# Optimization experiments

Hardware: AMD Instinct MI355X
Metric: run time of the kernel (lower is better)

Reference implementation:

```python
import jax, jax.numpy as jnp
import numpy as np

L, T, D, H, NC = 4, 2, 128, 8, 7
DH = D // H
DFF = 4 * D
EPS = 1e-5


def _ln(x, w, b):
    m = jnp.mean(x, axis=-1, keepdims=True)
    v = jnp.mean((x - m) ** 2, axis=-1, keepdims=True)
    return (x - m) / jnp.sqrt(v + EPS) * w + b


def setup_inputs() -> dict:
    key = jax.random.key(0)
    ks = jax.random.split(key, 16)
    s = 0.02
    inp = {
        "x": jax.random.normal(ks[0], (65536, 1, 2 * D), dtype=jnp.float32),
        "token_proj_w": jax.random.normal(ks[1], (T * D, T * D), dtype=jnp.float32) * s,
        "token_proj_b": jnp.zeros((T * D,), jnp.float32),
        "pos_emb": jax.random.normal(ks[2], (1, T, D), dtype=jnp.float32),
        "qkv_w": jax.random.normal(ks[3], (L, 3 * D, D), dtype=jnp.float32) * s,
        "qkv_b": jnp.zeros((L, 3 * D), jnp.float32),
        "out_w": jax.random.normal(ks[4], (L, D, D), dtype=jnp.float32) * s,
        "out_b": jnp.zeros((L, D), jnp.float32),
        "ln1_w": jnp.ones((L, D), jnp.float32),
        "ln1_b": jnp.zeros((L, D), jnp.float32),
        "ff1_w": jax.random.normal(ks[5], (L, DFF, D), dtype=jnp.float32) * s,
        "ff1_b": jnp.zeros((L, DFF), jnp.float32),
        "ff2_w": jax.random.normal(ks[6], (L, D, DFF), dtype=jnp.float32) * s,
        "ff2_b": jnp.zeros((L, D), jnp.float32),
        "ln2_w": jnp.ones((L, D), jnp.float32),
        "ln2_b": jnp.zeros((L, D), jnp.float32),
        "lnf_w": jnp.ones((D,), jnp.float32),
        "lnf_b": jnp.zeros((D,), jnp.float32),
        "cls_ln_w": jnp.ones((D,), jnp.float32),
        "cls_ln_b": jnp.zeros((D,), jnp.float32),
        "cls_w": jax.random.normal(ks[7], (NC, D), dtype=jnp.float32) * s,
        "cls_b": jnp.zeros((NC,), jnp.float32),
    }
    return inp


def _forward(x, token_proj_w, token_proj_b, pos_emb, qkv_w, qkv_b, out_w, out_b,
             ln1_w, ln1_b, ff1_w, ff1_b, ff2_w, ff2_b, ln2_w, ln2_b,
             lnf_w, lnf_b, cls_ln_w, cls_ln_b, cls_w, cls_b):
    x = jnp.squeeze(x, 1)                                  # [B, 256]
    B = x.shape[0]
    tok = x @ token_proj_w.T + token_proj_b                # [B, 256]
    tok = tok.reshape(B, T, D) + pos_emb                   # [B, 2, 128]
    scale = 1.0 / jnp.sqrt(jnp.float32(DH))
    for i in range(L):
        # --- self-attention (post-norm, as in nn.TransformerEncoderLayer) ---
        qkv = jnp.einsum('btd,ed->bte', tok, qkv_w[i]) + qkv_b[i]   # [B,T,3D]
        q, k, v = jnp.split(qkv, 3, axis=-1)
        q = q.reshape(B, T, H, DH)
        k = k.reshape(B, T, H, DH)
        v = v.reshape(B, T, H, DH)
        scores = jnp.einsum('bqhd,bkhd->bhqk', q, k) * scale
        attn = jax.nn.softmax(scores, axis=-1)
        o = jnp.einsum('bhqk,bkhd->bqhd', attn, v).reshape(B, T, D)
        o = jnp.einsum('btd,ed->bte', o, out_w[i]) + out_b[i]
        tok = _ln(tok + o, ln1_w[i], ln1_b[i])
        # --- FFN ---
        h = jnp.einsum('btd,fd->btf', tok, ff1_w[i]) + ff1_b[i]
        h = jax.nn.gelu(h, approximate=False)
        h = jnp.einsum('btf,df->btd', h, ff2_w[i]) + ff2_b[i]
        tok = _ln(tok + h, ln2_w[i], ln2_b[i])
    tok = _ln(tok, lnf_w, lnf_b)                           # final encoder norm
    pooled = jnp.mean(tok, axis=1)                         # [B, D]
    out = _ln(pooled, cls_ln_w, cls_ln_b)
    out = jax.nn.gelu(out, approximate=False)
    return out @ cls_w.T + cls_b                           # [B, 7]


def reference(x, token_proj_w, token_proj_b, pos_emb, qkv_w, qkv_b, out_w, out_b,
              ln1_w, ln1_b, ff1_w, ff1_b, ff2_w, ff2_b, ln2_w, ln2_b,
              lnf_w, lnf_b, cls_ln_w, cls_ln_b, cls_w, cls_b):
    return _forward(x, token_proj_w, token_proj_b, pos_emb, qkv_w, qkv_b, out_w, out_b,
                    ln1_w, ln1_b, ff1_w, ff1_b, ff2_w, ff2_b, ln2_w, ln2_b,
                    lnf_w, lnf_b, cls_ln_w, cls_ln_b, cls_w, cls_b)
```

## Files before the change

kernel.cpp:

```cpp
#include <hip/hip_runtime.h>


#define DEV static __device__ __forceinline__

typedef __attribute__((ext_vector_type(8))) short short8;
typedef __attribute__((ext_vector_type(4))) float f32x4;

#define BS    32
#define MROWS 64
#define PITCH 136
#define XP    272
#define LEPS  1e-5f

#define OFF_TPW  0
#define OFF_QKVW 65536
#define OFF_OUTW 262144
#define OFF_FF1W 327680
#define OFF_FF2W 589824
#define WS_ELEMS 851968

DEV unsigned short f2b(float f) {
  unsigned u = __float_as_uint(f);
  return (unsigned short)((u + 0x7fffu + ((u >> 16) & 1u)) >> 16);
}
DEV float b2f(unsigned short s) { return __uint_as_float((unsigned)s << 16); }

DEV f32x4 MFMA(short8 a, short8 b, f32x4 c) {
  return __builtin_amdgcn_mfma_f32_16x16x32_bf16(a, b, c, 0, 0, 0);
}

DEV float gelu_f(float x) {
  float u = 0.7978845608028654f * (x + 0.044715f * x * x * x);
  float e = __expf(2.0f * u);
  float t = 1.0f - 2.0f / (e + 1.0f);
  return 0.5f * x * (1.0f + t);
}

DEV short8 ldfrag(const unsigned short* tile, int rowBase, int kk, int lane) {
  return *(const short8*)(tile + (rowBase + (lane & 15)) * PITCH + kk * 32 + (lane >> 4) * 8);
}
DEV short8 ldfragX(const unsigned short* tile, int rowBase, int koff, int lane) {
  return *(const short8*)(tile + (rowBase + (lane & 15)) * XP + koff + (lane >> 4) * 8);
}
DEV short8 ldBg(const unsigned short* __restrict__ base, int pitch, int colBase,
                int koff, int kk, int lane) {
  return *(const short8*)(base + (size_t)(colBase + (lane & 15)) * pitch +
                          koff + kk * 32 + (lane >> 4) * 8);
}

DEV void ln_residual_write(f32x4 (&val)[2][4], const float* __restrict__ w,
                           const float* __restrict__ b, unsigned short* sTok,
                           float* sRedP, float* sRedF, int tid) {
  const int wave = tid >> 6, lane = tid & 63, g = lane >> 4, j = lane & 15;
  float ps[4][4], pq[4][4];
#pragma unroll
  for (int rt = 0; rt < 4; ++rt)
#pragma unroll
    for (int r = 0; r < 4; ++r) {
      float v0 = val[0][rt][r], v1 = val[1][rt][r];
      float s = v0 + v1, q = v0 * v0 + v1 * v1;
#pragma unroll
      for (int m = 1; m < 16; m <<= 1) {
        s += __shfl_xor(s, m, 16);
        q += __shfl_xor(q, m, 16);
      }
      ps[rt][r] = s; pq[rt][r] = q;
    }
  if (j == 0) {
#pragma unroll
    for (int rt = 0; rt < 4; ++rt)
#pragma unroll
      for (int r = 0; r < 4; ++r) {
        int row = rt * 16 + g * 4 + r;
        sRedP[row * 8 + wave * 2]     = ps[rt][r];
        sRedP[row * 8 + wave * 2 + 1] = pq[rt][r];
      }
  }
  __syncthreads();
  if (tid < 64) {
    float s = 0.f, q = 0.f;
#pragma unroll
    for (int wv = 0; wv < 4; ++wv) {
      s += sRedP[tid * 8 + wv * 2];
      q += sRedP[tid * 8 + wv * 2 + 1];
    }
    float mean = s * (1.f / 128.f);
    sRedF[tid * 2]     = mean;
    sRedF[tid * 2 + 1] = rsqrtf(q * (1.f / 128.f) - mean * mean + LEPS);
  }
  __syncthreads();
#pragma unroll
  for (int h = 0; h < 2; ++h) {
    int n = (h * 4 + wave) * 16 + j;
    float wn = w[n], bn = b[n];
#pragma unroll
    for (int rt = 0; rt < 4; ++rt)
#pragma unroll
      for (int r = 0; r < 4; ++r) {
        int row = rt * 16 + g * 4 + r;
        float mean = sRedF[row * 2], rstd = sRedF[row * 2 + 1];
        sTok[row * PITCH + n] = f2b((val[h][rt][r] - mean) * rstd * wn + bn);
      }
  }
  __syncthreads();
}

__global__ __launch_bounds__(256)
void prep_w(const float* __restrict__ tpw, const float* __restrict__ qkvw,
            const float* __restrict__ outw, const float* __restrict__ ff1w,
            const float* __restrict__ ff2w, unsigned short* __restrict__ wsb) {
  int i = blockIdx.x * 256 + threadIdx.x;
  if (i >= WS_ELEMS) return;
  float v;
  if (i < OFF_QKVW)      v = tpw[i - OFF_TPW];
  else if (i < OFF_OUTW) v = qkvw[i - OFF_QKVW];
  else if (i < OFF_FF1W) v = outw[i - OFF_OUTW];
  else if (i < OFF_FF2W) v = ff1w[i - OFF_FF1W];
  else                   v = ff2w[i - OFF_FF2W];
  wsb[i] = f2b(v);
}

__global__ __launch_bounds__(256, 2)
void tx_fused(const float* __restrict__ x, const unsigned short* __restrict__ wsb,
              const float* __restrict__ tpb, const float* __restrict__ pos,
              const float* __restrict__ qkvb, const float* __restrict__ outb,
              const float* __restrict__ ln1w, const float* __restrict__ ln1b,
              const float* __restrict__ ff1b, const float* __restrict__ ff2b,
              const float* __restrict__ ln2w, const float* __restrict__ ln2b,
              const float* __restrict__ lnfw, const float* __restrict__ lnfb,
              const float* __restrict__ clnw, const float* __restrict__ clnb,
              const float* __restrict__ cw, const float* __restrict__ cb,
              float* __restrict__ out) {
  __shared__ __align__(16) unsigned short sTok[MROWS * PITCH];
  __shared__ __align__(16) unsigned short sStage[MROWS * PITCH];
  __shared__ float sRedP[MROWS * 8];
  __shared__ float sRedF[MROWS * 2];

  const int tid  = threadIdx.x;
  const int wave = tid >> 6;
  const int lane = tid & 63;
  const int g = lane >> 4, j = lane & 15;
  const size_t s0 = (size_t)blockIdx.x * BS;

  const unsigned short* tpwB  = wsb + OFF_TPW;
  const unsigned short* qkvwB = wsb + OFF_QKVW;
  const unsigned short* outwB = wsb + OFF_OUTW;
  const unsigned short* ff1wB = wsb + OFF_FF1W;
  const unsigned short* ff2wB = wsb + OFF_FF2W;

  const f32x4 zero4 = {0.f, 0.f, 0.f, 0.f};

  {
#pragma unroll
    for (int it = 0; it < 2; ++it) {
      int idx = it * 256 + tid;
      int r = idx >> 4, s = idx & 15;
      const float4* p = (const float4*)(x + (s0 + r) * 256 + s * 16);
      float4 f0 = p[0], f1 = p[1], f2 = p[2], f3 = p[3];
      short8 lo, hi;
      lo[0] = (short)f2b(f0.x); lo[1] = (short)f2b(f0.y);
      lo[2] = (short)f2b(f0.z); lo[3] = (short)f2b(f0.w);
      lo[4] = (short)f2b(f1.x); lo[5] = (short)f2b(f1.y);
      lo[6] = (short)f2b(f1.z); lo[7] = (short)f2b(f1.w);
      hi[0] = (short)f2b(f2.x); hi[1] = (short)f2b(f2.y);
      hi[2] = (short)f2b(f2.z); hi[3] = (short)f2b(f2.w);
      hi[4] = (short)f2b(f3.x); hi[5] = (short)f2b(f3.y);
      hi[6] = (short)f2b(f3.z); hi[7] = (short)f2b(f3.w);
      *(short8*)(sStage + r * XP + s * 16)     = lo;
      *(short8*)(sStage + r * XP + s * 16 + 8) = hi;
    }
  }
  __syncthreads();

  f32x4 accTP[2][2][2];
#pragma unroll
  for (int nc = 0; nc < 2; ++nc)
#pragma unroll
    for (int h = 0; h < 2; ++h)
#pragma unroll
      for (int rt = 0; rt < 2; ++rt) accTP[nc][h][rt] = zero4;

#pragma unroll
  for (int kc = 0; kc < 2; ++kc)
#pragma unroll
    for (int nc = 0; nc < 2; ++nc)
#pragma unroll
      for (int h = 0; h < 2; ++h) {
        int cb = nc * 128 + (h * 4 + wave) * 16;
        short8 bf[4];
#pragma unroll
        for (int kk = 0; kk < 4; ++kk)
          bf[kk] = ldBg(tpwB, 256, cb, kc * 128, kk, lane);
#pragma unroll
        for (int rt = 0; rt < 2; ++rt)
#pragma unroll
          for (int kk = 0; kk < 4; ++kk)
            accTP[nc][h][rt] = MFMA(ldfragX(sStage, rt * 16, kc * 128 + kk * 32, lane),
                                    bf[kk], accTP[nc][h][rt]);
      }
  __syncthreads();
#pragma unroll
  for (int nc = 0; nc < 2; ++nc)
#pragma unroll
    for (int h = 0; h < 2; ++h) {
      int d = (h * 4 + wave) * 16 + j;
      float bias = tpb[nc * 128 + d] + pos[nc * 128 + d];
#pragma unroll
      for (int rt = 0; rt < 2; ++rt)
#pragma unroll
        for (int r = 0; r < 4; ++r) {
          int sm = rt * 16 + g * 4 + r;
          sTok[(2 * sm + nc) * PITCH + d] = f2b(accTP[nc][h][rt][r] + bias);
        }
    }
  __syncthreads();

  for (int li = 0; li < 4; ++li) {
    const unsigned short* qkvL = qkvwB + (size_t)li * 49152;
    const unsigned short* outL = outwB + (size_t)li * 16384;
    const unsigned short* ff1L = ff1wB + (size_t)li * 65536;
    const unsigned short* ff2L = ff2wB + (size_t)li * 65536;

    short8 aT[4][4];
#pragma unroll
    for (int rt = 0; rt < 4; ++rt)
#pragma unroll
      for (int kk = 0; kk < 4; ++kk) aT[rt][kk] = ldfrag(sTok, rt * 16, kk, lane);

    f32x4 acc[6][4];
#pragma unroll
    for (int a = 0; a < 6; ++a)
#pragma unroll
      for (int rt = 0; rt < 4; ++rt) acc[a][rt] = zero4;

#pragma unroll
    for (int nc = 0; nc < 3; ++nc)
#pragma unroll
      for (int h = 0; h < 2; ++h) {
        int cb = nc * 128 + (h * 4 + wave) * 16;
        short8 bf[4];
#pragma unroll
        for (int kk = 0; kk < 4; ++kk) bf[kk] = ldBg(qkvL, 128, cb, 0, kk, lane);
        int a = nc * 2 + h;
#pragma unroll
        for (int rt = 0; rt < 4; ++rt)
#pragma unroll
          for (int kk = 0; kk < 4; ++kk)
            acc[a][rt] = MFMA(aT[rt][kk], bf[kk], acc[a][rt]);
      }
#pragma unroll
    for (int a = 0; a < 6; ++a) {
      int nc = a >> 1, h = a & 1;
      float bv = qkvb[li * 384 + nc * 128 + (h * 4 + wave) * 16 + j];
#pragma unroll
      for (int rt = 0; rt < 4; ++rt) acc[a][rt] += bv;
    }

#pragma unroll
    for (int hh = 0; hh < 2; ++hh) {
      int head = hh * 4 + wave;
#pragma unroll
      for (int rt = 0; rt < 4; ++rt)
#pragma unroll
        for (int sp = 0; sp < 2; ++sp) {
          int r0 = sp * 2, r1 = r0 + 1;
          float q0 = acc[hh][rt][r0],     q1 = acc[hh][rt][r1];
          float k0 = acc[2 + hh][rt][r0], k1 = acc[2 + hh][rt][r1];
          float s00 = q0 * k0, s01 = q0 * k1, s10 = q1 * k0, s11 = q1 * k1;
#pragma unroll
          for (int m = 1; m < 16; m <<= 1) {
            s00 += __shfl_xor(s00, m, 16);
            s01 += __shfl_xor(s01, m, 16);
            s10 += __shfl_xor(s10, m, 16);
            s11 += __shfl_xor(s11, m, 16);
          }
          s00 *= 0.25f; s01 *= 0.25f; s10 *= 0.25f; s11 *= 0.25f;
          float m0 = fmaxf(s00, s01), m1 = fmaxf(s10, s11);
          float e00 = __expf(s00 - m0), e01 = __expf(s01 - m0);
          float e10 = __expf(s10 - m1), e11 = __expf(s11 - m1);
          float i0 = 1.f / (e00 + e01), i1 = 1.f / (e10 + e11);
          float v0 = acc[4 + hh][rt][r0], v1 = acc[4 + hh][rt][r1];
          float o0 = (e00 * v0 + e01 * v1) * i0;
          float o1 = (e10 * v0 + e11 * v1) * i1;
          int rowb = rt * 16 + g * 4 + r0;
          int col  = head * 16 + j;
          sStage[rowb * PITCH + col]       = f2b(o0);
          sStage[(rowb + 1) * PITCH + col] = f2b(o1);
        }
    }
    __syncthreads();

    short8 aO[4][4];
#pragma unroll
    for (int rt = 0; rt < 4; ++rt)
#pragma unroll
      for (int kk = 0; kk < 4; ++kk) aO[rt][kk] = ldfrag(sStage, rt * 16, kk, lane);

    f32x4 accO[2][4];
#pragma unroll
    for (int h = 0; h < 2; ++h)
#pragma unroll
      for (int rt = 0; rt < 4; ++rt) accO[h][rt] = zero4;
#pragma unroll
    for (int h = 0; h < 2; ++h) {
      int cb = (h * 4 + wave) * 16;
      short8 bf[4];
#pragma unroll
      for (int kk = 0; kk < 4; ++kk) bf[kk] = ldBg(outL, 128, cb, 0, kk, lane);
#pragma unroll
      for (int rt = 0; rt < 4; ++rt)
#pragma unroll
        for (int kk = 0; kk < 4; ++kk)
          accO[h][rt] = MFMA(aO[rt][kk], bf[kk], accO[h][rt]);
    }
#pragma unroll
    for (int h = 0; h < 2; ++h) {
      int n = (h * 4 + wave) * 16 + j;
      float ob = outb[li * 128 + n];
#pragma unroll
      for (int rt = 0; rt < 4; ++rt)
#pragma unroll
        for (int r = 0; r < 4; ++r) {
          int row = rt * 16 + g * 4 + r;
          accO[h][rt][r] += ob + b2f(sTok[row * PITCH + n]);
        }
    }
    ln_residual_write(accO, ln1w + li * 128, ln1b + li * 128, sTok, sRedP, sRedF, tid);

    short8 aF[4][4];
#pragma unroll
    for (int rt = 0; rt < 4; ++rt)
#pragma unroll
      for (int kk = 0; kk < 4; ++kk) aF[rt][kk] = ldfrag(sTok, rt * 16, kk, lane);

    f32x4 accF[2][4];
#pragma unroll
    for (int h = 0; h < 2; ++h)
#pragma unroll
      for (int rt = 0; rt < 4; ++rt) accF[h][rt] = zero4;

    for (int fc = 0; fc < 4; ++fc) {
      f32x4 hacc[2][4];
#pragma unroll
      for (int h = 0; h < 2; ++h)
#pragma unroll
        for (int rt = 0; rt < 4; ++rt) hacc[h][rt] = zero4;
#pragma unroll
      for (int h = 0; h < 2; ++h) {
        int cb = fc * 128 + (h * 4 + wave) * 16;
        short8 bf[4];
#pragma unroll
        for (int kk = 0; kk < 4; ++kk) bf[kk] = ldBg(ff1L, 128, cb, 0, kk, lane);
#pragma unroll
        for (int rt = 0; rt < 4; ++rt)
#pragma unroll
          for (int kk = 0; kk < 4; ++kk)
            hacc[h][rt] = MFMA(aF[rt][kk], bf[kk], hacc[h][rt]);
      }
      __syncthreads();
#pragma unroll
      for (int h = 0; h < 2; ++h) {
        int nl = (h * 4 + wave) * 16 + j;
        float bb = ff1b[li * 512 + fc * 128 + nl];
#pragma unroll
        for (int rt = 0; rt < 4; ++rt)
#pragma unroll
          for (int r = 0; r < 4; ++r) {
            float hv = gelu_f(hacc[h][rt][r] + bb);
            sStage[(rt * 16 + g * 4 + r) * PITCH + nl] = f2b(hv);
          }
      }
      __syncthreads();
      short8 aH[4][4];
#pragma unroll
      for (int rt = 0; rt < 4; ++rt)
#pragma unroll
        for (int kk = 0; kk < 4; ++kk) aH[rt][kk] = ldfrag(sStage, rt * 16, kk, lane);
#pragma unroll
      for (int h = 0; h < 2; ++h) {
        int cb = (h * 4 + wave) * 16;
        short8 bf[4];
#pragma unroll
        for (int kk = 0; kk < 4; ++kk)
          bf[kk] = ldBg(ff2L, 512, cb, fc * 128, kk, lane);
#pragma unroll
        for (int rt = 0; rt < 4; ++rt)
#pragma unroll
          for (int kk = 0; kk < 4; ++kk)
            accF[h][rt] = MFMA(aH[rt][kk], bf[kk], accF[h][rt]);
      }
    }
#pragma unroll
    for (int h = 0; h < 2; ++h) {
      int n = (h * 4 + wave) * 16 + j;
      float fb = ff2b[li * 128 + n];
#pragma unroll
      for (int rt = 0; rt < 4; ++rt)
#pragma unroll
        for (int r = 0; r < 4; ++r) {
          int row = rt * 16 + g * 4 + r;
          accF[h][rt][r] += fb + b2f(sTok[row * PITCH + n]);
        }
    }
    ln_residual_write(accF, ln2w + li * 128, ln2b + li * 128, sTok, sRedP, sRedF, tid);
  }

  {
    int row = tid >> 2, q4 = tid & 3;
    const unsigned short* rp = sTok + row * PITCH + q4 * 32;
    float vb[32];
    float s = 0.f, sq = 0.f;
#pragma unroll
    for (int t8 = 0; t8 < 4; ++t8) {
      short8 v = *(const short8*)(rp + t8 * 8);
#pragma unroll
      for (int e = 0; e < 8; ++e) {
        float f = b2f((unsigned short)v[e]);
        vb[t8 * 8 + e] = f; s += f; sq += f * f;
      }
    }
    s  += __shfl_xor(s, 1, 4);  s  += __shfl_xor(s, 2, 4);
    sq += __shfl_xor(sq, 1, 4); sq += __shfl_xor(sq, 2, 4);
    float mean = s * (1.f / 128.f);
    float rstd = rsqrtf(sq * (1.f / 128.f) - mean * mean + LEPS);
    unsigned short* wp = sTok + row * PITCH + q4 * 32;
#pragma unroll
    for (int c = 0; c < 32; ++c) {
      int col = q4 * 32 + c;
      wp[c] = f2b((vb[c] - mean) * rstd * lnfw[col] + lnfb[col]);
    }
  }
  __syncthreads();
  {
    int sIdx = tid >> 3, oct = tid & 7;
    float pv[16];
    float s = 0.f, sq = 0.f;
#pragma unroll
    for (int t8 = 0; t8 < 2; ++t8) {
      short8 va  = *(const short8*)(sTok + (2 * sIdx) * PITCH + oct * 16 + t8 * 8);
      short8 vb2 = *(const short8*)(sTok + (2 * sIdx + 1) * PITCH + oct * 16 + t8 * 8);
#pragma unroll
      for (int e = 0; e < 8; ++e) {
        float f = 0.5f * (b2f((unsigned short)va[e]) + b2f((unsigned short)vb2[e]));
        pv[t8 * 8 + e] = f; s += f; sq += f * f;
      }
    }
    s  += __shfl_xor(s, 1, 8);  s  += __shfl_xor(s, 2, 8);  s  += __shfl_xor(s, 4, 8);
    sq += __shfl_xor(sq, 1, 8); sq += __shfl_xor(sq, 2, 8); sq += __shfl_xor(sq, 4, 8);
    float mean = s * (1.f / 128.f);
    float rstd = rsqrtf(sq * (1.f / 128.f) - mean * mean + LEPS);
    float gv[16];
#pragma unroll
    for (int c = 0; c < 16; ++c) {
      int col = oct * 16 + c;
      gv[c] = gelu_f((pv[c] - mean) * rstd * clnw[col] + clnb[col]);
    }
#pragma unroll
    for (int cc = 0; cc < 7; ++cc) {
      float p = 0.f;
#pragma unroll
      for (int c = 0; c < 16; ++c) p += gv[c] * cw[cc * 128 + oct * 16 + c];
      p += __shfl_xor(p, 1, 8); p += __shfl_xor(p, 2, 8); p += __shfl_xor(p, 4, 8);
      if (oct == 0) out[(s0 + sIdx) * 7 + cc] = p + cb[cc];
    }
  }
}

extern "C" void kernel_launch(void* const* d_in, const int* in_sizes, int n_in,
                              void* d_out, int out_size, void* d_ws, size_t ws_size,
                              hipStream_t stream) {
  (void)n_in; (void)out_size; (void)ws_size;
  const float* x    = (const float*)d_in[0];
  const float* tpw  = (const float*)d_in[1];
  const float* tpb  = (const float*)d_in[2];
  const float* pos  = (const float*)d_in[3];
  const float* qkvw = (const float*)d_in[4];
  const float* qkvb = (const float*)d_in[5];
  const float* outw = (const float*)d_in[6];
  const float* outb = (const float*)d_in[7];
  const float* ln1w = (const float*)d_in[8];
  const float* ln1b = (const float*)d_in[9];
  const float* ff1w = (const float*)d_in[10];
  const float* ff1b = (const float*)d_in[11];
  const float* ff2w = (const float*)d_in[12];
  const float* ff2b = (const float*)d_in[13];
  const float* ln2w = (const float*)d_in[14];
  const float* ln2b = (const float*)d_in[15];
  const float* lnfw = (const float*)d_in[16];
  const float* lnfb = (const float*)d_in[17];
  const float* clnw = (const float*)d_in[18];
  const float* clnb = (const float*)d_in[19];
  const float* cw   = (const float*)d_in[20];
  const float* cb   = (const float*)d_in[21];
  unsigned short* wsb = (unsigned short*)d_ws;

  int B = in_sizes[0] / 256;

  hipLaunchKernelGGL(prep_w, dim3((WS_ELEMS + 255) / 256), dim3(256), 0, stream,
                     tpw, qkvw, outw, ff1w, ff2w, wsb);
  hipLaunchKernelGGL(tx_fused, dim3(B / BS), dim3(256), 0, stream,
                     x, wsb, tpb, pos, qkvb, outb, ln1w, ln1b, ff1b, ff2b,
                     ln2w, ln2b, lnfw, lnfb, clnw, clnb, cw, cb, (float*)d_out);
}
```

Baseline: 719.3 us.

## Prefetch weight fragments ahead of use, double-buffer FFN staging, raise MFMA priority

Issues the global loads for the next GEMM's weight fragments (QKV, out-proj, FF1, FF2) before the preceding LN, attention or GELU phases, so their latency overlaps other work. The FFN hidden staging buffer alternates between two LDS buffers, which removes one of the two barriers per FFN chunk, and the fc loop is now fully unrolled. MFMA sections are wrapped in s_setprio to favour the matrix-issuing waves. The extra LDS buffer and the prefetched register fragments raise LDS use and register pressure, which could reduce occupancy below the 2-blocks-per-CU launch bound or cause spills.

New measurement: 768.3 us. 1.07x slower.

```diff
diff --git a/kernel.cpp b/kernel.cpp
--- a/kernel.cpp
+++ b/kernel.cpp
@@ -133,6 +133,7 @@
               float* __restrict__ out) {
   __shared__ __align__(16) unsigned short sTok[MROWS * PITCH];
   __shared__ __align__(16) unsigned short sStage[MROWS * PITCH];
+  __shared__ __align__(16) unsigned short sStage2[MROWS * PITCH];
   __shared__ float sRedP[MROWS * 8];
   __shared__ float sRedF[MROWS * 2];
 
@@ -180,6 +181,7 @@
 #pragma unroll
       for (int rt = 0; rt < 2; ++rt) accTP[nc][h][rt] = zero4;
 
+  __builtin_amdgcn_s_setprio(1);
 #pragma unroll
   for (int kc = 0; kc < 2; ++kc)
 #pragma unroll
@@ -198,6 +200,14 @@
             accTP[nc][h][rt] = MFMA(ldfragX(sStage, rt * 16, kc * 128 + kk * 32, lane),
                                     bf[kk], accTP[nc][h][rt]);
       }
+  __builtin_amdgcn_s_setprio(0);
+  short8 bfQ[2][4];
+#pragma unroll
+  for (int h = 0; h < 2; ++h)
+#pragma unroll
+    for (int kk = 0; kk < 4; ++kk)
+      bfQ[h][kk] = ldBg(qkvwB, 128, (h * 4 + wave) * 16, 0, kk, lane);
+
   __syncthreads();
 #pragma unroll
   for (int nc = 0; nc < 2; ++nc)
@@ -233,14 +243,20 @@
 #pragma unroll
       for (int rt = 0; rt < 4; ++rt) acc[a][rt] = zero4;
 
+    __builtin_amdgcn_s_setprio(1);
 #pragma unroll
     for (int nc = 0; nc < 3; ++nc)
 #pragma unroll
       for (int h = 0; h < 2; ++h) {
-        int cb = nc * 128 + (h * 4 + wave) * 16;
         short8 bf[4];
-#pragma unroll
-        for (int kk = 0; kk < 4; ++kk) bf[kk] = ldBg(qkvL, 128, cb, 0, kk, lane);
+        if (nc == 0) {
+#pragma unroll
+          for (int kk = 0; kk < 4; ++kk) bf[kk] = bfQ[h][kk];
+        } else {
+          int cb = nc * 128 + (h * 4 + wave) * 16;
+#pragma unroll
+          for (int kk = 0; kk < 4; ++kk) bf[kk] = ldBg(qkvL, 128, cb, 0, kk, lane);
+        }
         int a = nc * 2 + h;
 #pragma unroll
         for (int rt = 0; rt < 4; ++rt)
@@ -248,6 +264,7 @@
           for (int kk = 0; kk < 4; ++kk)
             acc[a][rt] = MFMA(aT[rt][kk], bf[kk], acc[a][rt]);
       }
+    __builtin_amdgcn_s_setprio(0);
 #pragma unroll
     for (int a = 0; a < 6; ++a) {
       int nc = a >> 1, h = a & 1;
@@ -255,6 +272,13 @@
 #pragma unroll
       for (int rt = 0; rt < 4; ++rt) acc[a][rt] += bv;
     }
+
+    short8 bfO[2][4];
+#pragma unroll
+    for (int h = 0; h < 2; ++h)
+#pragma unroll
+      for (int kk = 0; kk < 4; ++kk)
+        bfO[h][kk] = ldBg(outL, 128, (h * 4 + wave) * 16, 0, kk, lane);
 
 #pragma unroll
     for (int hh = 0; hh < 2; ++hh) {
@@ -301,18 +325,15 @@
     for (int h = 0; h < 2; ++h)
 #pragma unroll
       for (int rt = 0; rt < 4; ++rt) accO[h][rt] = zero4;
-#pragma unroll
-    for (int h = 0; h < 2; ++h) {
-      int cb = (h * 4 + wave) * 16;
-      short8 bf[4];
-#pragma unroll
-      for (int kk = 0; kk < 4; ++kk) bf[kk] = ldBg(outL, 128, cb, 0, kk, lane);
+    __builtin_amdgcn_s_setprio(1);
+#pragma unroll
+    for (int h = 0; h < 2; ++h)
 #pragma unroll
       for (int rt = 0; rt < 4; ++rt)
 #pragma unroll
         for (int kk = 0; kk < 4; ++kk)
-          accO[h][rt] = MFMA(aO[rt][kk], bf[kk], accO[h][rt]);
-    }
+          accO[h][rt] = MFMA(aO[rt][kk], bfO[h][kk], accO[h][rt]);
+    __builtin_amdgcn_s_setprio(0);
 #pragma unroll
     for (int h = 0; h < 2; ++h) {
       int n = (h * 4 + wave) * 16 + j;
@@ -325,6 +346,13 @@
           accO[h][rt][r] += ob + b2f(sTok[row * PITCH + n]);
         }
     }
+    short8 bfF[2][4];
+#pragma unroll
+    for (int h = 0; h < 2; ++h)
+#pragma unroll
+      for (int kk = 0; kk < 4; ++kk)
+        bfF[h][kk] = ldBg(ff1L, 128, (h * 4 + wave) * 16, 0, kk, lane);
+
     ln_residual_write(accO, ln1w + li * 128, ln1b + li * 128, sTok, sRedP, sRedF, tid);
 
     short8 aF[4][4];
@@ -339,25 +367,29 @@
 #pragma unroll
       for (int rt = 0; rt < 4; ++rt) accF[h][rt] = zero4;
 
+#pragma unroll
     for (int fc = 0; fc < 4; ++fc) {
+      unsigned short* hb = (fc & 1) ? sStage2 : sStage;
       f32x4 hacc[2][4];
 #pragma unroll
       for (int h = 0; h < 2; ++h)
 #pragma unroll
         for (int rt = 0; rt < 4; ++rt) hacc[h][rt] = zero4;
-#pragma unroll
-      for (int h = 0; h < 2; ++h) {
-        int cb = fc * 128 + (h * 4 + wave) * 16;
-        short8 bf[4];
-#pragma unroll
-        for (int kk = 0; kk < 4; ++kk) bf[kk] = ldBg(ff1L, 128, cb, 0, kk, lane);
+      __builtin_amdgcn_s_setprio(1);
+#pragma unroll
+      for (int h = 0; h < 2; ++h)
 #pragma unroll
         for (int rt = 0; rt < 4; ++rt)
 #pragma unroll
           for (int kk = 0; kk < 4; ++kk)
-            hacc[h][rt] = MFMA(aF[rt][kk], bf[kk], hacc[h][rt]);
-      }
-      __syncthreads();
+            hacc[h][rt] = MFMA(aF[rt][kk], bfF[h][kk], hacc[h][rt]);
+      __builtin_amdgcn_s_setprio(0);
+      short8 bf2[2][4];
+#pragma unroll
+      for (int h = 0; h < 2; ++h)
+#pragma unroll
+        for (int kk = 0; kk < 4; ++kk)
+          bf2[h][kk] = ldBg(ff2L, 512, (h * 4 + wave) * 16, fc * 128, kk, lane);
 #pragma unroll
       for (int h = 0; h < 2; ++h) {
         int nl = (h * 4 + wave) * 16 + j;
@@ -367,7 +399,7 @@
 #pragma unroll
           for (int r = 0; r < 4; ++r) {
             float hv = gelu_f(hacc[h][rt][r] + bb);
-            sStage[(rt * 16 + g * 4 + r) * PITCH + nl] = f2b(hv);
+            hb[(rt * 16 + g * 4 + r) * PITCH + nl] = f2b(hv);
           }
       }
       __syncthreads();
@@ -375,20 +407,23 @@
 #pragma unroll
       for (int rt = 0; rt < 4; ++rt)
 #pragma unroll
-        for (int kk = 0; kk < 4; ++kk) aH[rt][kk] = ldfrag(sStage, rt * 16, kk, lane);
-#pragma unroll
-      for (int h = 0; h < 2; ++h) {
-        int cb = (h * 4 + wave) * 16;
-        short8 bf[4];
-#pragma unroll
-        for (int kk = 0; kk < 4; ++kk)
-          bf[kk] = ldBg(ff2L, 512, cb, fc * 128, kk, lane);
+        for (int kk = 0; kk < 4; ++kk) aH[rt][kk] = ldfrag(hb, rt * 16, kk, lane);
+      if (fc < 3) {
+#pragma unroll
+        for (int h = 0; h < 2; ++h)
+#pragma unroll
+          for (int kk = 0; kk < 4; ++kk)
+            bfF[h][kk] = ldBg(ff1L, 128, (fc + 1) * 128 + (h * 4 + wave) * 16, 0, kk, lane);
+      }
+      __builtin_amdgcn_s_setprio(1);
+#pragma unroll
+      for (int h = 0; h < 2; ++h)
 #pragma unroll
         for (int rt = 0; rt < 4; ++rt)
 #pragma unroll
           for (int kk = 0; kk < 4; ++kk)
-            accF[h][rt] = MFMA(aH[rt][kk], bf[kk], accF[h][rt]);
-      }
+            accF[h][rt] = MFMA(aH[rt][kk], bf2[h][kk], accF[h][rt]);
+      __builtin_amdgcn_s_setprio(0);
     }
 #pragma unroll
     for (int h = 0; h < 2; ++h) {
@@ -401,6 +436,13 @@
           int row = rt * 16 + g * 4 + r;
           accF[h][rt][r] += fb + b2f(sTok[row * PITCH + n]);
         }
+    }
+    if (li < 3) {
+#pragma unroll
+      for (int h = 0; h < 2; ++h)
+#pragma unroll
+        for (int kk = 0; kk < 4; ++kk)
+          bfQ[h][kk] = ldBg(qkvL + 49152, 128, (h * 4 + wave) * 16, 0, kk, lane);
     }
     ln_residual_write(accF, ln2w + li * 128, ln2b + li * 128, sTok, sRedP, sRedF, tid);
   }
```

## Double-buffer FFN hidden staging, fold LN stats into all threads, add MFMA priority hints

Applied to the files above, without the earlier changes.

The FFN hidden-activation staging now ping-pongs between two LDS buffers, which removes one block barrier per FFN chunk. The layernorm helper has every thread reduce the per-wave partial sums itself instead of a separate 64-thread pass, dropping a second barrier and the sRedF buffer. s_setprio raises wave priority around the MFMA loops so matrix work can overlap other waves' memory and ALU phases. The cost is an extra 17KB of LDS per block, which may reduce occupancy, plus redundant reduction reads in every thread.

Measured after the change: 752.8 us. 4.7% more time.

```diff
diff --git a/kernel.cpp b/kernel.cpp
--- a/kernel.cpp
+++ b/kernel.cpp
@@ -50,7 +50,7 @@
 
 DEV void ln_residual_write(f32x4 (&val)[2][4], const float* __restrict__ w,
                            const float* __restrict__ b, unsigned short* sTok,
-                           float* sRedP, float* sRedF, int tid) {
+                           float* sRedP, int tid) {
   const int wave = tid >> 6, lane = tid & 63, g = lane >> 4, j = lane & 15;
   float ps[4][4], pq[4][4];
 #pragma unroll
@@ -77,31 +77,31 @@
       }
   }
   __syncthreads();
-  if (tid < 64) {
-    float s = 0.f, q = 0.f;
-#pragma unroll
-    for (int wv = 0; wv < 4; ++wv) {
-      s += sRedP[tid * 8 + wv * 2];
-      q += sRedP[tid * 8 + wv * 2 + 1];
-    }
-    float mean = s * (1.f / 128.f);
-    sRedF[tid * 2]     = mean;
-    sRedF[tid * 2 + 1] = rsqrtf(q * (1.f / 128.f) - mean * mean + LEPS);
-  }
-  __syncthreads();
+  float wn[2], bn[2];
 #pragma unroll
   for (int h = 0; h < 2; ++h) {
     int n = (h * 4 + wave) * 16 + j;
-    float wn = w[n], bn = b[n];
-#pragma unroll
-    for (int rt = 0; rt < 4; ++rt)
-#pragma unroll
-      for (int r = 0; r < 4; ++r) {
-        int row = rt * 16 + g * 4 + r;
-        float mean = sRedF[row * 2], rstd = sRedF[row * 2 + 1];
-        sTok[row * PITCH + n] = f2b((val[h][rt][r] - mean) * rstd * wn + bn);
-      }
+    wn[h] = w[n]; bn[h] = b[n];
   }
+#pragma unroll
+  for (int rt = 0; rt < 4; ++rt)
+#pragma unroll
+    for (int r = 0; r < 4; ++r) {
+      int row = rt * 16 + g * 4 + r;
+      float s = 0.f, q = 0.f;
+#pragma unroll
+      for (int wv = 0; wv < 4; ++wv) {
+        s += sRedP[row * 8 + wv * 2];
+        q += sRedP[row * 8 + wv * 2 + 1];
+      }
+      float mean = s * (1.f / 128.f);
+      float rstd = rsqrtf(q * (1.f / 128.f) - mean * mean + LEPS);
+#pragma unroll
+      for (int h = 0; h < 2; ++h) {
+        int n = (h * 4 + wave) * 16 + j;
+        sTok[row * PITCH + n] = f2b((val[h][rt][r] - mean) * rstd * wn[h] + bn[h]);
+      }
+    }
   __syncthreads();
 }
 
@@ -133,8 +133,8 @@
               float* __restrict__ out) {
   __shared__ __align__(16) unsigned short sTok[MROWS * PITCH];
   __shared__ __align__(16) unsigned short sStage[MROWS * PITCH];
+  __shared__ __align__(16) unsigned short sStage2[MROWS * PITCH];
   __shared__ float sRedP[MROWS * 8];
-  __shared__ float sRedF[MROWS * 2];
 
   const int tid  = threadIdx.x;
   const int wave = tid >> 6;
@@ -180,6 +180,7 @@
 #pragma unroll
       for (int rt = 0; rt < 2; ++rt) accTP[nc][h][rt] = zero4;
 
+  __builtin_amdgcn_s_setprio(1);
 #pragma unroll
   for (int kc = 0; kc < 2; ++kc)
 #pragma unroll
@@ -198,6 +199,7 @@
             accTP[nc][h][rt] = MFMA(ldfragX(sStage, rt * 16, kc * 128 + kk * 32, lane),
                                     bf[kk], accTP[nc][h][rt]);
       }
+  __builtin_amdgcn_s_setprio(0);
   __syncthreads();
 #pragma unroll
   for (int nc = 0; nc < 2; ++nc)
@@ -233,6 +235,7 @@
 #pragma unroll
       for (int rt = 0; rt < 4; ++rt) acc[a][rt] = zero4;
 
+    __builtin_amdgcn_s_setprio(1);
 #pragma unroll
     for (int nc = 0; nc < 3; ++nc)
 #pragma unroll
@@ -248,6 +251,7 @@
           for (int kk = 0; kk < 4; ++kk)
             acc[a][rt] = MFMA(aT[rt][kk], bf[kk], acc[a][rt]);
       }
+    __builtin_amdgcn_s_setprio(0);
 #pragma unroll
     for (int a = 0; a < 6; ++a) {
       int nc = a >> 1, h = a & 1;
@@ -301,6 +305,7 @@
     for (int h = 0; h < 2; ++h)
 #pragma unroll
       for (int rt = 0; rt < 4; ++rt) accO[h][rt] = zero4;
+    __builtin_amdgcn_s_setprio(1);
 #pragma unroll
     for (int h = 0; h < 2; ++h) {
       int cb = (h * 4 + wave) * 16;
@@ -313,6 +318,7 @@
         for (int kk = 0; kk < 4; ++kk)
           accO[h][rt] = MFMA(aO[rt][kk], bf[kk], accO[h][rt]);
     }
+    __builtin_amdgcn_s_setprio(0);
 #pragma unroll
     for (int h = 0; h < 2; ++h) {
       int n = (h * 4 + wave) * 16 + j;
@@ -325,7 +331,7 @@
           accO[h][rt][r] += ob + b2f(sTok[row * PITCH + n]);
         }
     }
-    ln_residual_write(accO, ln1w + li * 128, ln1b + li * 128, sTok, sRedP, sRedF, tid);
+    ln_residual_write(accO, ln1w + li * 128, ln1b + li * 128, sTok, sRedP, tid);
 
     short8 aF[4][4];
 #pragma unroll
@@ -339,12 +345,15 @@
 #pragma unroll
       for (int rt = 0; rt < 4; ++rt) accF[h][rt] = zero4;
 
+#pragma unroll
     for (int fc = 0; fc < 4; ++fc) {
+      unsigned short* hb = (fc & 1) ? sStage2 : sStage;
       f32x4 hacc[2][4];
 #pragma unroll
       for (int h = 0; h < 2; ++h)
 #pragma unroll
         for (int rt = 0; rt < 4; ++rt) hacc[h][rt] = zero4;
+      __builtin_amdgcn_s_setprio(1);
 #pragma unroll
       for (int h = 0; h < 2; ++h) {
         int cb = fc * 128 + (h * 4 + wave) * 16;
@@ -357,7 +366,7 @@
           for (int kk = 0; kk < 4; ++kk)
             hacc[h][rt] = MFMA(aF[rt][kk], bf[kk], hacc[h][rt]);
       }
-      __syncthreads();
+      __builtin_amdgcn_s_setprio(0);
 #pragma unroll
       for (int h = 0; h < 2; ++h) {
         int nl = (h * 4 + wave) * 16 + j;
@@ -367,7 +376,7 @@
 #pragma unroll
           for (int r = 0; r < 4; ++r) {
             float hv = gelu_f(hacc[h][rt][r] + bb);
-            sStage[(rt * 16 + g * 4 + r) * PITCH + nl] = f2b(hv);
+            hb[(rt * 16 + g * 4 + r) * PITCH + nl] = f2b(hv);
           }
       }
       __syncthreads();
@@ -375,7 +384,8 @@
 #pragma unroll
       for (int rt = 0; rt < 4; ++rt)
 #pragma unroll
-        for (int kk = 0; kk < 4; ++kk) aH[rt][kk] = ldfrag(sStage, rt * 16, kk, lane);
+        for (int kk = 0; kk < 4; ++kk) aH[rt][kk] = ldfrag(hb, rt * 16, kk, lane);
+      __builtin_amdgcn_s_setprio(1);
 #pragma unroll
       for (int h = 0; h < 2; ++h) {
         int cb = (h * 4 + wave) * 16;
@@ -389,6 +399,7 @@
           for (int kk = 0; kk < 4; ++kk)
             accF[h][rt] = MFMA(aH[rt][kk], bf[kk], accF[h][rt]);
       }
+      __builtin_amdgcn_s_setprio(0);
     }
 #pragma unroll
     for (int h = 0; h < 2; ++h) {
@@ -402,7 +413,7 @@
           accF[h][rt][r] += fb + b2f(sTok[row * PITCH + n]);
         }
     }
-    ln_residual_write(accF, ln2w + li * 128, ln2b + li * 128, sTok, sRedP, sRedF, tid);
+    ln_residual_write(accF, ln2w + li * 128, ln2b + li * 128, sTok, sRedP, tid);
   }
 
   {
```

## Split row tiles into halves to cut register pressure and raise occupancy

Applied to the files above, without the earlier changes.

Each GEMM phase (QKV plus attention, out-projection, FF1, FF2) now processes the 64-row tile in two halves of 32 rows, so fewer A-fragments and accumulators are live at once. The launch bound goes from 2 to 3 blocks per CU to take advantage of the lower register use. In exchange, weight B-fragments are loaded from global memory twice per phase. FF1 now reloads sTok fragments each chunk, which adds a barrier per chunk.

New measurement: 871.4 us. 1.21x slower.

```diff
diff --git a/kernel.cpp b/kernel.cpp
--- a/kernel.cpp
+++ b/kernel.cpp
@@ -120,7 +120,7 @@
   wsb[i] = f2b(v);
 }
 
-__global__ __launch_bounds__(256, 2)
+__global__ __launch_bounds__(256, 3)
 void tx_fused(const float* __restrict__ x, const unsigned short* __restrict__ wsb,
               const float* __restrict__ tpb, const float* __restrict__ pos,
               const float* __restrict__ qkvb, const float* __restrict__ outb,
@@ -221,97 +221,109 @@
     const unsigned short* ff1L = ff1wB + (size_t)li * 65536;
     const unsigned short* ff2L = ff2wB + (size_t)li * 65536;
 
-    short8 aT[4][4];
-#pragma unroll
-    for (int rt = 0; rt < 4; ++rt)
-#pragma unroll
-      for (int kk = 0; kk < 4; ++kk) aT[rt][kk] = ldfrag(sTok, rt * 16, kk, lane);
-
-    f32x4 acc[6][4];
-#pragma unroll
-    for (int a = 0; a < 6; ++a)
-#pragma unroll
-      for (int rt = 0; rt < 4; ++rt) acc[a][rt] = zero4;
-
-#pragma unroll
-    for (int nc = 0; nc < 3; ++nc)
+#pragma unroll
+    for (int half = 0; half < 2; ++half) {
+      const int rtb = half * 2;
+      short8 aT[2][4];
+#pragma unroll
+      for (int p = 0; p < 2; ++p)
+#pragma unroll
+        for (int kk = 0; kk < 4; ++kk)
+          aT[p][kk] = ldfrag(sTok, (rtb + p) * 16, kk, lane);
+
+      f32x4 acc2[6][2];
+#pragma unroll
+      for (int a = 0; a < 6; ++a)
+#pragma unroll
+        for (int p = 0; p < 2; ++p) acc2[a][p] = zero4;
+
+#pragma unroll
+      for (int nc = 0; nc < 3; ++nc)
+#pragma unroll
+        for (int h = 0; h < 2; ++h) {
+          int cb = nc * 128 + (h * 4 + wave) * 16;
+          short8 bf[4];
+#pragma unroll
+          for (int kk = 0; kk < 4; ++kk) bf[kk] = ldBg(qkvL, 128, cb, 0, kk, lane);
+          int a = nc * 2 + h;
+#pragma unroll
+          for (int p = 0; p < 2; ++p)
+#pragma unroll
+            for (int kk = 0; kk < 4; ++kk)
+              acc2[a][p] = MFMA(aT[p][kk], bf[kk], acc2[a][p]);
+        }
+#pragma unroll
+      for (int a = 0; a < 6; ++a) {
+        int nc = a >> 1, h = a & 1;
+        float bv = qkvb[li * 384 + nc * 128 + (h * 4 + wave) * 16 + j];
+#pragma unroll
+        for (int p = 0; p < 2; ++p) acc2[a][p] += bv;
+      }
+
+#pragma unroll
+      for (int hh = 0; hh < 2; ++hh) {
+        int head = hh * 4 + wave;
+#pragma unroll
+        for (int p = 0; p < 2; ++p) {
+          int rt = rtb + p;
+#pragma unroll
+          for (int sp = 0; sp < 2; ++sp) {
+            int r0 = sp * 2, r1 = r0 + 1;
+            float q0 = acc2[hh][p][r0],     q1 = acc2[hh][p][r1];
+            float k0 = acc2[2 + hh][p][r0], k1 = acc2[2 + hh][p][r1];
+            float s00 = q0 * k0, s01 = q0 * k1, s10 = q1 * k0, s11 = q1 * k1;
+#pragma unroll
+            for (int m = 1; m < 16; m <<= 1) {
+              s00 += __shfl_xor(s00, m, 16);
+              s01 += __shfl_xor(s01, m, 16);
+              s10 += __shfl_xor(s10, m, 16);
+              s11 += __shfl_xor(s11, m, 16);
+            }
+            s00 *= 0.25f; s01 *= 0.25f; s10 *= 0.25f; s11 *= 0.25f;
+            float m0 = fmaxf(s00, s01), m1 = fmaxf(s10, s11);
+            float e00 = __expf(s00 - m0), e01 = __expf(s01 - m0);
+            float e10 = __expf(s10 - m1), e11 = __expf(s11 - m1);
+            float i0 = 1.f / (e00 + e01), i1 = 1.f / (e10 + e11);
+            float v0 = acc2[4 + hh][p][r0], v1 = acc2[4 + hh][p][r1];
+            float o0 = (e00 * v0 + e01 * v1) * i0;
+            float o1 = (e10 * v0 + e11 * v1) * i1;
+            int rowb = rt * 16 + g * 4 + r0;
+            int col  = head * 16 + j;
+            sStage[rowb * PITCH + col]       = f2b(o0);
+            sStage[(rowb + 1) * PITCH + col] = f2b(o1);
+          }
+        }
+      }
+    }
+    __syncthreads();
+
+    f32x4 accO[2][4];
+#pragma unroll
+    for (int h = 0; h < 2; ++h)
+#pragma unroll
+      for (int rt = 0; rt < 4; ++rt) accO[h][rt] = zero4;
+
+#pragma unroll
+    for (int half = 0; half < 2; ++half) {
+      const int rtb = half * 2;
+      short8 aO[2][4];
+#pragma unroll
+      for (int p = 0; p < 2; ++p)
+#pragma unroll
+        for (int kk = 0; kk < 4; ++kk)
+          aO[p][kk] = ldfrag(sStage, (rtb + p) * 16, kk, lane);
 #pragma unroll
       for (int h = 0; h < 2; ++h) {
-        int cb = nc * 128 + (h * 4 + wave) * 16;
+        int cb = (h * 4 + wave) * 16;
         short8 bf[4];
 #pragma unroll
-        for (int kk = 0; kk < 4; ++kk) bf[kk] = ldBg(qkvL, 128, cb, 0, kk, lane);
-        int a = nc * 2 + h;
-#pragma unroll
-        for (int rt = 0; rt < 4; ++rt)
+        for (int kk = 0; kk < 4; ++kk) bf[kk] = ldBg(outL, 128, cb, 0, kk, lane);
+#pragma unroll
+        for (int p = 0; p < 2; ++p)
 #pragma unroll
           for (int kk = 0; kk < 4; ++kk)
-            acc[a][rt] = MFMA(aT[rt][kk], bf[kk], acc[a][rt]);
-      }
-#pragma unroll
-    for (int a = 0; a < 6; ++a) {
-      int nc = a >> 1, h = a & 1;
-      float bv = qkvb[li * 384 + nc * 128 + (h * 4 + wave) * 16 + j];
-#pragma unroll
-      for (int rt = 0; rt < 4; ++rt) acc[a][rt] += bv;
-    }
-
-#pragma unroll
-    for (int hh = 0; hh < 2; ++hh) {
-      int head = hh * 4 + wave;
-#pragma unroll
-      for (int rt = 0; rt < 4; ++rt)
-#pragma unroll
-        for (int sp = 0; sp < 2; ++sp) {
-          int r0 = sp * 2, r1 = r0 + 1;
-          float q0 = acc[hh][rt][r0],     q1 = acc[hh][rt][r1];
-          float k0 = acc[2 + hh][rt][r0], k1 = acc[2 + hh][rt][r1];
-          float s00 = q0 * k0, s01 = q0 * k1, s10 = q1 * k0, s11 = q1 * k1;
-#pragma unroll
-          for (int m = 1; m < 16; m <<= 1) {
-            s00 += __shfl_xor(s00, m, 16);
-            s01 += __shfl_xor(s01, m, 16);
-            s10 += __shfl_xor(s10, m, 16);
-            s11 += __shfl_xor(s11, m, 16);
-          }
-          s00 *= 0.25f; s01 *= 0.25f; s10 *= 0.25f; s11 *= 0.25f;
-          float m0 = fmaxf(s00, s01), m1 = fmaxf(s10, s11);
-          float e00 = __expf(s00 - m0), e01 = __expf(s01 - m0);
-          float e10 = __expf(s10 - m1), e11 = __expf(s11 - m1);
-          float i0 = 1.f / (e00 + e01), i1 = 1.f / (e10 + e11);
-          float v0 = acc[4 + hh][rt][r0], v1 = acc[4 + hh][rt][r1];
-          float o0 = (e00 * v0 + e01 * v1) * i0;
-          float o1 = (e10 * v0 + e11 * v1) * i1;
-          int rowb = rt * 16 + g * 4 + r0;
-          int col  = head * 16 + j;
-          sStage[rowb * PITCH + col]       = f2b(o0);
-          sStage[(rowb + 1) * PITCH + col] = f2b(o1);
-        }
-    }
-    __syncthreads();
-
-    short8 aO[4][4];
-#pragma unroll
-    for (int rt = 0; rt < 4; ++rt)
-#pragma unroll
-      for (int kk = 0; kk < 4; ++kk) aO[rt][kk] = ldfrag(sStage, rt * 16, kk, lane);
-
-    f32x4 accO[2][4];
-#pragma unroll
-    for (int h = 0; h < 2; ++h)
-#pragma unroll
-      for (int rt = 0; rt < 4; ++rt) accO[h][rt] = zero4;
-#pragma unroll
-    for (int h = 0; h < 2; ++h) {
-      int cb = (h * 4 + wave) * 16;
-      short8 bf[4];
-#pragma unroll
-      for (int kk = 0; kk < 4; ++kk) bf[kk] = ldBg(outL, 128, cb, 0, kk, lane);
-#pragma unroll
-      for (int rt = 0; rt < 4; ++rt)
-#pragma unroll
-        for (int kk = 0; kk < 4; ++kk)
-          accO[h][rt] = MFMA(aO[rt][kk], bf[kk], accO[h][rt]);
+            accO[h][rtb + p] = MFMA(aO[p][kk], bf[kk], accO[h][rtb + p]);
+      }
     }
 #pragma unroll
     for (int h = 0; h < 2; ++h) {
@@ -327,12 +339,6 @@
     }
     ln_residual_write(accO, ln1w + li * 128, ln1b + li * 128, sTok, sRedP, sRedF, tid);
 
-    short8 aF[4][4];
-#pragma unroll
-    for (int rt = 0; rt < 4; ++rt)
-#pragma unroll
-      for (int kk = 0; kk < 4; ++kk) aF[rt][kk] = ldfrag(sTok, rt * 16, kk, lane);
-
     f32x4 accF[2][4];
 #pragma unroll
     for (int h = 0; h < 2; ++h)
@@ -340,54 +346,69 @@
       for (int rt = 0; rt < 4; ++rt) accF[h][rt] = zero4;
 
     for (int fc = 0; fc < 4; ++fc) {
-      f32x4 hacc[2][4];
-#pragma unroll
-      for (int h = 0; h < 2; ++h)
-#pragma unroll
-        for (int rt = 0; rt < 4; ++rt) hacc[h][rt] = zero4;
-#pragma unroll
-      for (int h = 0; h < 2; ++h) {
-        int cb = fc * 128 + (h * 4 + wave) * 16;
-        short8 bf[4];
-#pragma unroll
-        for (int kk = 0; kk < 4; ++kk) bf[kk] = ldBg(ff1L, 128, cb, 0, kk, lane);
-#pragma unroll
-        for (int rt = 0; rt < 4; ++rt)
+      __syncthreads();
+#pragma unroll
+      for (int half = 0; half < 2; ++half) {
+        const int rtb = half * 2;
+        short8 aF[2][4];
+#pragma unroll
+        for (int p = 0; p < 2; ++p)
 #pragma unroll
           for (int kk = 0; kk < 4; ++kk)
-            hacc[h][rt] = MFMA(aF[rt][kk], bf[kk], hacc[h][rt]);
+            aF[p][kk] = ldfrag(sTok, (rtb + p) * 16, kk, lane);
+        f32x4 hacc[2][2];
+#pragma unroll
+        for (int h = 0; h < 2; ++h)
+#pragma unroll
+          for (int p = 0; p < 2; ++p) hacc[h][p] = zero4;
+#pragma unroll
+        for (int h = 0; h < 2; ++h) {
+          int cb = fc * 128 + (h * 4 + wave) * 16;
+          short8 bf[4];
+#pragma unroll
+          for (int kk = 0; kk < 4; ++kk) bf[kk] = ldBg(ff1L, 128, cb, 0, kk, lane);
+#pragma unroll
+          for (int p = 0; p < 2; ++p)
+#pragma unroll
+            for (int kk = 0; kk < 4; ++kk)
+              hacc[h][p] = MFMA(aF[p][kk], bf[kk], hacc[h][p]);
+        }
+#pragma unroll
+        for (int h = 0; h < 2; ++h) {
+          int nl = (h * 4 + wave) * 16 + j;
+          float bb = ff1b[li * 512 + fc * 128 + nl];
+#pragma unroll
+          for (int p = 0; p < 2; ++p)
+#pragma unroll
+            for (int r = 0; r < 4; ++r) {
+              float hv = gelu_f(hacc[h][p][r] + bb);
+              sStage[((rtb + p) * 16 + g * 4 + r) * PITCH + nl] = f2b(hv);
+            }
+        }
       }
       __syncthreads();
 #pragma unroll
-      for (int h = 0; h < 2; ++h) {
-        int nl = (h * 4 + wave) * 16 + j;
-        float bb = ff1b[li * 512 + fc * 128 + nl];
-#pragma unroll
-        for (int rt = 0; rt < 4; ++rt)
-#pragma unroll
-          for (int r = 0; r < 4; ++r) {
-            float hv = gelu_f(hacc[h][rt][r] + bb);
-            sStage[(rt * 16 + g * 4 + r) * PITCH + nl] = f2b(hv);
-          }
-      }
-      __syncthreads();
-      short8 aH[4][4];
-#pragma unroll
-      for (int rt = 0; rt < 4; ++rt)
-#pragma unroll
-        for (int kk = 0; kk < 4; ++kk) aH[rt][kk] = ldfrag(sStage, rt * 16, kk, lane);
-#pragma unroll
-      for (int h = 0; h < 2; ++h) {
-        int cb = (h * 4 + wave) * 16;
-        short8 bf[4];
-#pragma unroll
-        for (int kk = 0; kk < 4; ++kk)
-          bf[kk] = ldBg(ff2L, 512, cb, fc * 128, kk, lane);
-#pragma unroll
-        for (int rt = 0; rt < 4; ++rt)
+      for (int half = 0; half < 2; ++half) {
+        const int rtb = half * 2;
+        short8 aH[2][4];
+#pragma unroll
+        for (int p = 0; p < 2; ++p)
 #pragma unroll
           for (int kk = 0; kk < 4; ++kk)
-            accF[h][rt] = MFMA(aH[rt][kk], bf[kk], accF[h][rt]);
+            aH[p][kk] = ldfrag(sStage, (rtb + p) * 16, kk, lane);
+#pragma unroll
+        for (int h = 0; h < 2; ++h) {
+          int cb = (h * 4 + wave) * 16;
+          short8 bf[4];
+#pragma unroll
+          for (int kk = 0; kk < 4; ++kk)
+            bf[kk] = ldBg(ff2L, 512, cb, fc * 128, kk, lane);
+#pragma unroll
+          for (int p = 0; p < 2; ++p)
+#pragma unroll
+            for (int kk = 0; kk < 4; ++kk)
+              accF[h][rtb + p] = MFMA(aH[p][kk], bf[kk], accF[h][rtb + p]);
+        }
       }
     }
 #pragma unroll
```
